# Kernel tuning notes

Measured on AMD Instinct MI355X. Metric: run time of the kernel, lower is better.

Reference implementation:

```python
import jax, jax.numpy as jnp
import numpy as np
from jax.scipy.linalg import expm

NUM_QUBITS = 10
D = 2 ** NUM_QUBITS  # 1024
B, S = 8, 4096


def setup_inputs() -> dict:
    key = jax.random.key(0)
    k_x, k_mr, k_mi = jax.random.split(key, 3)
    inputs = jax.random.normal(k_x, (B, S, D), dtype=jnp.float32)
    M_real = 0.1 * jax.random.normal(k_mr, (D, D), dtype=jnp.float32)
    M_imag = 0.1 * jax.random.normal(k_mi, (D, D), dtype=jnp.float32)
    bias = jnp.zeros((D,), dtype=jnp.float32)
    qubit_gate = jnp.ones((D,), dtype=jnp.float32)
    return {"inputs": inputs, "M_real": M_real, "M_imag": M_imag,
            "bias": bias, "qubit_gate": qubit_gate}


def _l2_normalize(x, axis=-1, eps=1e-12):
    # matches tf.linalg.l2_normalize: x * rsqrt(max(sum(x^2), eps))
    ss = jnp.sum(jnp.square(x), axis=axis, keepdims=True)
    return x * jax.lax.rsqrt(jnp.maximum(ss, eps))


def reference(inputs, M_real, M_imag, bias, qubit_gate):
    norm_inputs = _l2_normalize(inputs, axis=-1)
    A = M_real - M_real.T  # skew-symmetric -> expm(A) is orthogonal
    Bm = M_imag - M_imag.T
    U = expm(A) @ expm(Bm)  # [D, D]
    transformed = jnp.einsum('bsd,de->bse', norm_inputs, U) + bias
    measured = jnp.square(transformed)
    gate_probs = jax.nn.softmax(qubit_gate)  # [D]
    gated_output = measured * gate_probs
    return gated_output, gate_probs
```

## Files before the change

### kernel.cpp

```cpp
#include <hip/hip_runtime.h>


typedef unsigned int u32;
typedef unsigned short u16;
typedef __attribute__((ext_vector_type(8))) short short8;
typedef __attribute__((ext_vector_type(4))) float f32x4;

#define GLOBAL_AS __attribute__((address_space(1)))
#define LDS_AS    __attribute__((address_space(3)))

constexpr int D = 1024;
constexpr float EXPM_SCALE = 1.0f / 8.0f;

__device__ __forceinline__ u16 f2bf(float f) {
  union { float f; u32 u; } v; v.f = f;
  u32 r = (v.u + 0x7FFFu + ((v.u >> 16) & 1u)) >> 16;
  return (u16)r;
}
__device__ __forceinline__ float bf2f(u16 u) {
  union { u32 u; float f; } v; v.u = ((u32)u) << 16;
  return v.f;
}

__device__ __forceinline__ void g2l16(const void* g, void* l) {
  __builtin_amdgcn_global_load_lds((const GLOBAL_AS u32*)g, (LDS_AS u32*)l,
                                   16, 0, 0);
}

__device__ void norm_row(const float* __restrict__ x, u16* __restrict__ Xn,
                         int r, int tid, float* s4) {
  const float4 v = ((const float4*)(x + (size_t)r * D))[tid];
  float ss = v.x * v.x + v.y * v.y + v.z * v.z + v.w * v.w;
  for (int o = 32; o; o >>= 1) ss += __shfl_down(ss, o);
  if ((tid & 63) == 0) s4[tid >> 6] = ss;
  __syncthreads();
  const float tot = s4[0] + s4[1] + s4[2] + s4[3];
  const float inv = rsqrtf(fmaxf(tot, 1e-12f));
  ushort4 o4;
  o4.x = f2bf(v.x * inv); o4.y = f2bf(v.y * inv);
  o4.z = f2bf(v.z * inv); o4.w = f2bf(v.w * inv);
  ((ushort4*)(Xn + (size_t)r * D))[tid] = o4;
}

struct SkewParams {
  const float *Mr, *Mi;
  u16 *X0, *X1;
  const float* x;
  u16* Xn;
  int row0;
};
__global__ __launch_bounds__(256) void skew_norm_kernel(SkewParams p) {
  __shared__ __align__(16) float t2[64][67];
  const int bid = blockIdx.x, tid = threadIdx.x;
  if (bid >= 512) {
    norm_row(p.x, p.Xn, p.row0 + bid - 512, tid, &t2[0][0]);
    return;
  }
  const int z = bid >> 8, t = bid & 255;
  const float* M = z ? p.Mi : p.Mr;
  u16* X = z ? p.X1 : p.X0;
  const int bi = t >> 4, bj = t & 15;
  const int r0 = tid >> 4, c0 = (tid & 15) * 4;
  float4 own[4];
#pragma unroll
  for (int i = 0; i < 4; ++i) {
    const int r = i * 16 + r0;
    own[i] = *(const float4*)(M + (size_t)(bi * 64 + r) * D + bj * 64 + c0);
    const float4 tr =
        *(const float4*)(M + (size_t)(bj * 64 + r) * D + bi * 64 + c0);
    t2[r][c0 + 0] = tr.x; t2[r][c0 + 1] = tr.y;
    t2[r][c0 + 2] = tr.z; t2[r][c0 + 3] = tr.w;
  }
  __syncthreads();
#pragma unroll
  for (int i = 0; i < 4; ++i) {
    const int r = i * 16 + r0;
    const float o[4] = {own[i].x, own[i].y, own[i].z, own[i].w};
    ushort4 hv;
    u16* hp = (u16*)&hv;
#pragma unroll
    for (int j = 0; j < 4; ++j)
      hp[j] = f2bf((o[j] - t2[c0 + j][r]) * EXPM_SCALE);
    *(ushort4*)(X + (size_t)(bi * 64 + r) * D + bj * 64 + c0) = hv;
  }
}

struct CJob {
  const u16 *A, *B;
  const float* C;
  u16 *Dst, *DT;
  float alpha;
};
struct GNParams {
  CJob jobs[4];
  int njobs;
  const float* x;
  u16* Xn;
  int row0;
};
__global__ __launch_bounds__(256) void gemm_norm_kernel(GNParams p) {
  __shared__ __align__(16) u16 ldsA[2][64 * 64];
  __shared__ __align__(16) u16 ldsB[2][64 * 64];
  const int bid = blockIdx.x, tid = threadIdx.x;
  if (bid >= p.njobs) {
    norm_row(p.x, p.Xn, p.row0 + bid - p.njobs, tid, (float*)&ldsA[0][0]);
    return;
  }
  const CJob jb = p.jobs[bid >> 8];
  const int bi = (bid >> 4) & 15, bj = bid & 15;
  const int w = tid >> 6, lane = tid & 63;
  const int wr = w >> 1, wc = w & 1;
  f32x4 acc[2][2];
#pragma unroll
  for (int m = 0; m < 2; ++m)
#pragma unroll
    for (int n = 0; n < 2; ++n) acc[m][n] = f32x4{0.f, 0.f, 0.f, 0.f};
  const int r_l = lane >> 3, c_l = lane & 7;

  auto stage = [&](int buf, int kt) {
    const int k0 = kt * 64;
#pragma unroll
    for (int pp = 0; pp < 2; ++pp) {
      const int row = pp * 32 + w * 8 + r_l;
      const int chunk = c_l ^ (row & 7);
      g2l16(jb.A + (size_t)(bi * 64 + row) * D + k0 + chunk * 8,
            (char*)&ldsA[buf][0] + pp * 4096 + w * 1024);
      g2l16(jb.B + (size_t)(bj * 64 + row) * D + k0 + chunk * 8,
            (char*)&ldsB[buf][0] + pp * 4096 + w * 1024);
    }
  };

  stage(0, 0);
  __syncthreads();
  int buf = 0;
  for (int kt = 0; kt < 16; ++kt) {
    if (kt < 15) stage(buf ^ 1, kt + 1);
#pragma unroll
    for (int h = 0; h < 2; ++h) {
      const int kk = h * 32 + (lane >> 4) * 8;
      short8 a[2], b[2];
#pragma unroll
      for (int m = 0; m < 2; ++m) {
        const int row = wr * 32 + m * 16 + (lane & 15);
        const int off = row * 128 + ((kk * 2) ^ ((row & 7) << 4));
        a[m] = *(const short8*)((const char*)&ldsA[buf][0] + off);
      }
#pragma unroll
      for (int n = 0; n < 2; ++n) {
        const int row = wc * 32 + n * 16 + (lane & 15);
        const int off = row * 128 + ((kk * 2) ^ ((row & 7) << 4));
        b[n] = *(const short8*)((const char*)&ldsB[buf][0] + off);
      }
#pragma unroll
      for (int m = 0; m < 2; ++m)
#pragma unroll
        for (int n = 0; n < 2; ++n)
          acc[m][n] = __builtin_amdgcn_mfma_f32_16x16x32_bf16(
              a[m], b[n], acc[m][n], 0, 0, 0);
    }
    __syncthreads();
    buf ^= 1;
  }
  const int or0 = bi * 64 + wr * 32, oc0 = bj * 64 + wc * 32;
#pragma unroll
  for (int m = 0; m < 2; ++m)
#pragma unroll
    for (int n = 0; n < 2; ++n) {
      const int row0 = or0 + m * 16 + (lane >> 4) * 4;
      const int col = oc0 + n * 16 + (lane & 15);
      ushort4 dv;
      u16* dp = (u16*)&dv;
#pragma unroll
      for (int r = 0; r < 4; ++r) {
        float v = acc[m][n][r] * jb.alpha;
        if (jb.C) v += jb.C[(size_t)(row0 + r) * D + col];
        dp[r] = f2bf(v);
        jb.Dst[(size_t)(row0 + r) * D + col] = dp[r];
      }
      if (jb.DT)
        *(ushort4*)(jb.DT + (size_t)col * D + row0) = dv;
    }
}

struct BQParams {
  const u16 *X[2], *X2[2], *X3[2], *X4[2];
  float* q0[2];
  u16* q1t[2];
  const float* qg;
  float* gate_out;
  const float* x;
  u16* Xn;
  int row0;
};
__global__ __launch_bounds__(256) void buildq_norm_kernel(BQParams p) {
  __shared__ __align__(16) float red[16];
  const int bid = blockIdx.x, tid = threadIdx.x;
  if (bid > 512) {
    norm_row(p.x, p.Xn, p.row0 + bid - 513, tid, red);
    return;
  }
  if (bid == 512) {
    const float4 v = ((const float4*)p.qg)[tid];
    float mx = fmaxf(fmaxf(v.x, v.y), fmaxf(v.z, v.w));
#pragma unroll
    for (int o = 32; o; o >>= 1) mx = fmaxf(mx, __shfl_xor(mx, o));
    if ((tid & 63) == 0) red[tid >> 6] = mx;
    __syncthreads();
    const float M = fmaxf(fmaxf(red[0], red[1]), fmaxf(red[2], red[3]));
    __syncthreads();
    const float e0 = __expf(v.x - M), e1 = __expf(v.y - M),
                e2 = __expf(v.z - M), e3 = __expf(v.w - M);
    float s = e0 + e1 + e2 + e3;
#pragma unroll
    for (int o = 32; o; o >>= 1) s += __shfl_xor(s, o);
    if ((tid & 63) == 0) red[tid >> 6] = s;
    __syncthreads();
    const float S = red[0] + red[1] + red[2] + red[3];
    const float4 o4 = {e0 / S, e1 / S, e2 / S, e3 / S};
    ((float4*)p.gate_out)[tid] = o4;
    return;
  }
  const size_t idx0 = ((size_t)bid * 256 + tid) * 8;
  const int i = (int)(idx0 >> 10), j0 = (int)(idx0 & 1023);
#pragma unroll
  for (int m = 0; m < 2; ++m) {
    const short8 xv = *(const short8*)(p.X[m] + idx0);
    const short8 x2v = *(const short8*)(p.X2[m] + idx0);
    const short8 x3v = *(const short8*)(p.X3[m] + idx0);
    const short8 x4v = *(const short8*)(p.X4[m] + idx0);
    float q0o[8];
    short8 q1o;
#pragma unroll
    for (int k = 0; k < 8; ++k) {
      const float d = (i == (j0 + k)) ? 1.f : 0.f;
      const float x = bf2f((u16)xv[k]);
      const float x2 = bf2f((u16)x2v[k]);
      const float x3 = bf2f((u16)x3v[k]);
      const float x4 = bf2f((u16)x4v[k]);
      q0o[k] = d + x + x2 * 0.5f + x3 * (1.f / 6.f);
      q1o[k] = (short)f2bf(d * (1.f / 24.f) - x * (1.f / 120.f) +
                           x2 * (1.f / 720.f) - x3 * (1.f / 5040.f) +
                           x4 * (1.f / 40320.f));
    }
#pragma unroll
    for (int k = 0; k < 8; ++k) p.q0[m][idx0 + k] = q0o[k];
    *(short8*)(p.q1t[m] + idx0) = q1o;
  }
}

__global__ __launch_bounds__(512, 1) void main_gemm_kernel(
    const u16* __restrict__ Xn, const u16* __restrict__ Wm,
    const float* __restrict__ bias, const float* __restrict__ gate,
    float* __restrict__ out) {
  const int tid = threadIdx.x;
  const int wid = tid >> 6, lane = tid & 63;
  const int wr = wid >> 2, wc = wid & 3;
  __shared__ u16 ldsA[2][256 * 64];
  __shared__ u16 ldsB[2][256 * 64];
  f32x4 acc[8][4];
#pragma unroll
  for (int m = 0; m < 8; ++m)
#pragma unroll
    for (int n = 0; n < 4; ++n) acc[m][n] = f32x4{0.f, 0.f, 0.f, 0.f};

  const int bi = blockIdx.x, bj = blockIdx.y;
  const int r8 = tid >> 3;
  const int c_l = tid & 7;

  auto stage = [&](int buf, int kt) {
    const int k0 = kt * 64;
#pragma unroll
    for (int p = 0; p < 4; ++p) {
      const int row = p * 64 + r8;
      const int chunk = c_l ^ (row & 7);
      g2l16(Xn + (size_t)(bi * 256 + row) * D + k0 + chunk * 8,
            (u16*)((char*)&ldsA[buf][0] + p * 8192 + wid * 1024));
      g2l16(Wm + (size_t)(bj * 256 + row) * D + k0 + chunk * 8,
            (u16*)((char*)&ldsB[buf][0] + p * 8192 + wid * 1024));
    }
  };

  stage(0, 0);
  __syncthreads();
  int buf = 0;
  for (int kt = 0; kt < 16; ++kt) {
    if (kt < 15) stage(buf ^ 1, kt + 1);
#pragma unroll
    for (int ks = 0; ks < 2; ++ks) {
      const int kk = ks * 32 + (lane >> 4) * 8;
      short8 a[8], b[4];
#pragma unroll
      for (int m = 0; m < 8; ++m) {
        const int row = wr * 128 + m * 16 + (lane & 15);
        const int off = row * 128 + ((kk * 2) ^ ((row & 7) << 4));
        a[m] = *(const short8*)((const char*)&ldsA[buf][0] + off);
      }
#pragma unroll
      for (int n = 0; n < 4; ++n) {
        const int row = wc * 64 + n * 16 + (lane & 15);
        const int off = row * 128 + ((kk * 2) ^ ((row & 7) << 4));
        b[n] = *(const short8*)((const char*)&ldsB[buf][0] + off);
      }
      __builtin_amdgcn_s_setprio(1);
#pragma unroll
      for (int m = 0; m < 8; ++m)
#pragma unroll
        for (int n = 0; n < 4; ++n)
          acc[m][n] = __builtin_amdgcn_mfma_f32_16x16x32_bf16(
              a[m], b[n], acc[m][n], 0, 0, 0);
      __builtin_amdgcn_s_setprio(0);
    }
    __syncthreads();
    buf ^= 1;
  }
  const int or0 = bi * 256 + wr * 128, oc0 = bj * 256 + wc * 64;
#pragma unroll
  for (int m = 0; m < 8; ++m)
#pragma unroll
    for (int n = 0; n < 4; ++n) {
      const int col = oc0 + n * 16 + (lane & 15);
      const float bc = bias[col], gc = gate[col];
#pragma unroll
      for (int r = 0; r < 4; ++r) {
        const int row = or0 + m * 16 + (lane >> 4) * 4 + r;
        const float t = acc[m][n][r] + bc;
        out[(size_t)row * D + col] = t * t * gc;
      }
    }
}

extern "C" void kernel_launch(void* const* d_in, const int* in_sizes, int n_in,
                              void* d_out, int out_size, void* d_ws,
                              size_t ws_size, hipStream_t stream) {
  (void)in_sizes; (void)n_in; (void)out_size; (void)ws_size;
  const float* inp = (const float*)d_in[0];
  const float* Mr = (const float*)d_in[1];
  const float* Mi = (const float*)d_in[2];
  const float* bias = (const float*)d_in[3];
  const float* qg = (const float*)d_in[4];
  float* out = (float*)d_out;
  float* gate_out = out + (size_t)32768 * 1024;

  char* ws = (char*)d_ws;
  u16* Xn = (u16*)ws;
  auto slot = [&](int m, int s) -> u16* {
    return (u16*)(ws + 67108864 + (size_t)m * 16777216 + (size_t)s * 2097152);
  };
  auto q0p = [&](int m) -> float* {
    return (float*)(ws + 67108864 + (size_t)m * 16777216 + 12582912);
  };
  u16* W = (u16*)(ws + 100663296);

  const int CH = 3641;
  int row0 = 0;

  {
    SkewParams sp{Mr, Mi, slot(0, 0), slot(1, 0), inp, Xn, row0};
    skew_norm_kernel<<<512 + CH, 256, 0, stream>>>(sp);
    row0 += CH;
  }
  GNParams gp{};
  gp.x = inp; gp.Xn = Xn;
  for (int m = 0; m < 2; ++m)
    gp.jobs[m] = CJob{slot(m, 0), slot(m, 0), nullptr, slot(m, 1), nullptr,
                      -1.f};
  gp.njobs = 512; gp.row0 = row0;
  gemm_norm_kernel<<<512 + CH, 256, 0, stream>>>(gp);
  row0 += CH;
  for (int m = 0; m < 2; ++m) {
    gp.jobs[m * 2 + 0] = CJob{slot(m, 1), slot(m, 0), nullptr, slot(m, 2),
                              nullptr, -1.f};
    gp.jobs[m * 2 + 1] = CJob{slot(m, 1), slot(m, 1), nullptr, slot(m, 3),
                              nullptr, 1.f};
  }
  gp.njobs = 1024; gp.row0 = row0;
  gemm_norm_kernel<<<1024 + CH, 256, 0, stream>>>(gp);
  row0 += CH;
  {
    BQParams bq{};
    for (int m = 0; m < 2; ++m) {
      bq.X[m] = slot(m, 0); bq.X2[m] = slot(m, 1);
      bq.X3[m] = slot(m, 2); bq.X4[m] = slot(m, 3);
      bq.q0[m] = q0p(m); bq.q1t[m] = slot(m, 4);
    }
    bq.qg = qg; bq.gate_out = gate_out;
    bq.x = inp; bq.Xn = Xn; bq.row0 = row0;
    buildq_norm_kernel<<<513 + CH, 256, 0, stream>>>(bq);
    row0 += CH;
  }
  for (int m = 0; m < 2; ++m)
    gp.jobs[m] = CJob{slot(m, 3), slot(m, 4), q0p(m), slot(m, 0), slot(m, 1),
                      1.f};
  gp.njobs = 512; gp.row0 = row0;
  gemm_norm_kernel<<<512 + CH, 256, 0, stream>>>(gp);
  row0 += CH;
  for (int m = 0; m < 2; ++m)
    gp.jobs[m] = CJob{slot(m, 0), slot(m, 1), nullptr, slot(m, 2), slot(m, 4),
                      1.f};
  gp.row0 = row0;
  gemm_norm_kernel<<<512 + CH, 256, 0, stream>>>(gp);
  row0 += CH;
  for (int m = 0; m < 2; ++m)
    gp.jobs[m] = CJob{slot(m, 2), slot(m, 4), nullptr, slot(m, 3), slot(m, 5),
                      1.f};
  gp.row0 = row0;
  gemm_norm_kernel<<<512 + CH, 256, 0, stream>>>(gp);
  row0 += CH;
  for (int m = 0; m < 2; ++m)
    gp.jobs[m] = CJob{slot(m, 3), slot(m, 5), nullptr, slot(m, 0), slot(m, 1),
                      1.f};
  gp.row0 = row0;
  gemm_norm_kernel<<<512 + CH, 256, 0, stream>>>(gp);
  row0 += CH;
  gp.jobs[0] = CJob{slot(1, 1), slot(0, 0), nullptr, W, nullptr, 1.f};
  gp.njobs = 256; gp.row0 = row0;
  gemm_norm_kernel<<<256 + (32768 - row0), 256, 0, stream>>>(gp);

  main_gemm_kernel<<<dim3(128, 4), 512, 0, stream>>>(Xn, W, bias, gate_out,
                                                     out);
}
```

Measured before the change: 243.8 us.

## Batch norm rows, fuse X^3/X^4 GEMMs with Q build, deepen main GEMM pipeline

Each norm block now normalizes 8 rows instead of one, so the side work riding along each launch shrinks to 512 blocks. The separate X^3/X^4 GEMM launch and the elementwise Q-building kernel are merged into one kernel that shares the A tile across both products and builds q0/q1t in the epilogue. The main GEMM moves from a double-buffered 64-wide K tile to a four-stage 32-wide K ring with explicit vmcnt waits and raw barriers, aiming to overlap global loads with MFMA. This drops one launch and hides more load latency, but adds register and LDS pressure in the fused kernel and relies on hand-written wait counts being correct.

New measurement: 236.0 us. 1.03x faster.

```diff
diff --git a/kernel.cpp b/kernel.cpp
--- a/kernel.cpp
+++ b/kernel.cpp
@@ -27,19 +27,41 @@
                                    16, 0, 0);
 }
 
-__device__ void norm_row(const float* __restrict__ x, u16* __restrict__ Xn,
-                         int r, int tid, float* s4) {
-  const float4 v = ((const float4*)(x + (size_t)r * D))[tid];
-  float ss = v.x * v.x + v.y * v.y + v.z * v.z + v.w * v.w;
-  for (int o = 32; o; o >>= 1) ss += __shfl_down(ss, o);
-  if ((tid & 63) == 0) s4[tid >> 6] = ss;
+#define WAITV(N)                                                   \
+  do {                                                             \
+    asm volatile("s_waitcnt vmcnt(" #N ")" ::: "memory");          \
+    __builtin_amdgcn_sched_barrier(0);                             \
+  } while (0)
+
+__device__ void norm_rows8(const float* __restrict__ x, u16* __restrict__ Xn,
+                           int r0, int tid, float* sred) {
+  float4 v[8];
+#pragma unroll
+  for (int i = 0; i < 8; ++i)
+    v[i] = ((const float4*)(x + (size_t)(r0 + i) * D))[tid];
+  float ss[8];
+#pragma unroll
+  for (int i = 0; i < 8; ++i)
+    ss[i] = v[i].x * v[i].x + v[i].y * v[i].y + v[i].z * v[i].z +
+            v[i].w * v[i].w;
+  for (int o = 32; o; o >>= 1)
+#pragma unroll
+    for (int i = 0; i < 8; ++i) ss[i] += __shfl_down(ss[i], o);
+  const int w = tid >> 6;
+  if ((tid & 63) == 0)
+#pragma unroll
+    for (int i = 0; i < 8; ++i) sred[i * 4 + w] = ss[i];
   __syncthreads();
-  const float tot = s4[0] + s4[1] + s4[2] + s4[3];
-  const float inv = rsqrtf(fmaxf(tot, 1e-12f));
-  ushort4 o4;
-  o4.x = f2bf(v.x * inv); o4.y = f2bf(v.y * inv);
-  o4.z = f2bf(v.z * inv); o4.w = f2bf(v.w * inv);
-  ((ushort4*)(Xn + (size_t)r * D))[tid] = o4;
+#pragma unroll
+  for (int i = 0; i < 8; ++i) {
+    const float tot =
+        sred[i * 4 + 0] + sred[i * 4 + 1] + sred[i * 4 + 2] + sred[i * 4 + 3];
+    const float inv = rsqrtf(fmaxf(tot, 1e-12f));
+    ushort4 o4;
+    o4.x = f2bf(v[i].x * inv); o4.y = f2bf(v[i].y * inv);
+    o4.z = f2bf(v[i].z * inv); o4.w = f2bf(v[i].w * inv);
+    ((ushort4*)(Xn + (size_t)(r0 + i) * D))[tid] = o4;
+  }
 }
 
 struct SkewParams {
@@ -53,7 +75,7 @@
   __shared__ __align__(16) float t2[64][67];
   const int bid = blockIdx.x, tid = threadIdx.x;
   if (bid >= 512) {
-    norm_row(p.x, p.Xn, p.row0 + bid - 512, tid, &t2[0][0]);
+    norm_rows8(p.x, p.Xn, p.row0 + (bid - 512) * 8, tid, &t2[0][0]);
     return;
   }
   const int z = bid >> 8, t = bid & 255;
@@ -92,7 +114,7 @@
   float alpha;
 };
 struct GNParams {
-  CJob jobs[4];
+  CJob jobs[2];
   int njobs;
   const float* x;
   u16* Xn;
@@ -103,7 +125,8 @@
   __shared__ __align__(16) u16 ldsB[2][64 * 64];
   const int bid = blockIdx.x, tid = threadIdx.x;
   if (bid >= p.njobs) {
-    norm_row(p.x, p.Xn, p.row0 + bid - p.njobs, tid, (float*)&ldsA[0][0]);
+    norm_rows8(p.x, p.Xn, p.row0 + (bid - p.njobs) * 8, tid,
+               (float*)&ldsA[0][0]);
     return;
   }
   const CJob jb = p.jobs[bid >> 8];
@@ -182,27 +205,29 @@
     }
 }
 
-struct BQParams {
-  const u16 *X[2], *X2[2], *X3[2], *X4[2];
+struct X34Params {
+  const u16 *X[2], *X2[2];
+  u16 *X3[2], *X4[2], *q1t[2];
   float* q0[2];
-  u16* q1t[2];
   const float* qg;
   float* gate_out;
   const float* x;
   u16* Xn;
   int row0;
 };
-__global__ __launch_bounds__(256) void buildq_norm_kernel(BQParams p) {
-  __shared__ __align__(16) float red[16];
+__global__ __launch_bounds__(256) void x34q_norm_kernel(X34Params p) {
+  __shared__ __align__(16) u16 ldsA[2][64 * 64];
+  __shared__ __align__(16) u16 ldsB1[2][64 * 64];
+  __shared__ __align__(16) u16 ldsB2[2][64 * 64];
   const int bid = blockIdx.x, tid = threadIdx.x;
   if (bid > 512) {
-    norm_row(p.x, p.Xn, p.row0 + bid - 513, tid, red);
+    norm_rows8(p.x, p.Xn, p.row0 + (bid - 513) * 8, tid, (float*)&ldsA[0][0]);
     return;
   }
   if (bid == 512) {
+    float* red = (float*)&ldsA[0][0];
     const float4 v = ((const float4*)p.qg)[tid];
     float mx = fmaxf(fmaxf(v.x, v.y), fmaxf(v.z, v.w));
-#pragma unroll
     for (int o = 32; o; o >>= 1) mx = fmaxf(mx, __shfl_xor(mx, o));
     if ((tid & 63) == 0) red[tid >> 6] = mx;
     __syncthreads();
@@ -211,7 +236,6 @@
     const float e0 = __expf(v.x - M), e1 = __expf(v.y - M),
                 e2 = __expf(v.z - M), e3 = __expf(v.w - M);
     float s = e0 + e1 + e2 + e3;
-#pragma unroll
     for (int o = 32; o; o >>= 1) s += __shfl_xor(s, o);
     if ((tid & 63) == 0) red[tid >> 6] = s;
     __syncthreads();
@@ -220,32 +244,97 @@
     ((float4*)p.gate_out)[tid] = o4;
     return;
   }
-  const size_t idx0 = ((size_t)bid * 256 + tid) * 8;
-  const int i = (int)(idx0 >> 10), j0 = (int)(idx0 & 1023);
-#pragma unroll
-  for (int m = 0; m < 2; ++m) {
-    const short8 xv = *(const short8*)(p.X[m] + idx0);
-    const short8 x2v = *(const short8*)(p.X2[m] + idx0);
-    const short8 x3v = *(const short8*)(p.X3[m] + idx0);
-    const short8 x4v = *(const short8*)(p.X4[m] + idx0);
-    float q0o[8];
-    short8 q1o;
-#pragma unroll
-    for (int k = 0; k < 8; ++k) {
-      const float d = (i == (j0 + k)) ? 1.f : 0.f;
-      const float x = bf2f((u16)xv[k]);
-      const float x2 = bf2f((u16)x2v[k]);
-      const float x3 = bf2f((u16)x3v[k]);
-      const float x4 = bf2f((u16)x4v[k]);
-      q0o[k] = d + x + x2 * 0.5f + x3 * (1.f / 6.f);
-      q1o[k] = (short)f2bf(d * (1.f / 24.f) - x * (1.f / 120.f) +
-                           x2 * (1.f / 720.f) - x3 * (1.f / 5040.f) +
-                           x4 * (1.f / 40320.f));
-    }
-#pragma unroll
-    for (int k = 0; k < 8; ++k) p.q0[m][idx0 + k] = q0o[k];
-    *(short8*)(p.q1t[m] + idx0) = q1o;
-  }
+  const int mz = bid >> 8, t = bid & 255;
+  const int bi = t >> 4, bj = t & 15;
+  const u16* Ag = p.X2[mz];
+  const u16* B1g = p.X[mz];
+  const u16* B2g = p.X2[mz];
+  const int w = tid >> 6, lane = tid & 63;
+  const int wr = w >> 1, wc = w & 1;
+  f32x4 acc3[2][2], acc4[2][2];
+#pragma unroll
+  for (int m = 0; m < 2; ++m)
+#pragma unroll
+    for (int n = 0; n < 2; ++n) {
+      acc3[m][n] = f32x4{0.f, 0.f, 0.f, 0.f};
+      acc4[m][n] = f32x4{0.f, 0.f, 0.f, 0.f};
+    }
+  const int r_l = lane >> 3, c_l = lane & 7;
+
+  auto stage = [&](int buf, int kt) {
+    const int k0 = kt * 64;
+#pragma unroll
+    for (int pp = 0; pp < 2; ++pp) {
+      const int row = pp * 32 + w * 8 + r_l;
+      const int chunk = c_l ^ (row & 7);
+      g2l16(Ag + (size_t)(bi * 64 + row) * D + k0 + chunk * 8,
+            (char*)&ldsA[buf][0] + pp * 4096 + w * 1024);
+      g2l16(B1g + (size_t)(bj * 64 + row) * D + k0 + chunk * 8,
+            (char*)&ldsB1[buf][0] + pp * 4096 + w * 1024);
+      g2l16(B2g + (size_t)(bj * 64 + row) * D + k0 + chunk * 8,
+            (char*)&ldsB2[buf][0] + pp * 4096 + w * 1024);
+    }
+  };
+
+  stage(0, 0);
+  __syncthreads();
+  int buf = 0;
+  for (int kt = 0; kt < 16; ++kt) {
+    if (kt < 15) stage(buf ^ 1, kt + 1);
+#pragma unroll
+    for (int h = 0; h < 2; ++h) {
+      const int kk = h * 32 + (lane >> 4) * 8;
+      short8 a[2], b1[2], b2[2];
+#pragma unroll
+      for (int m = 0; m < 2; ++m) {
+        const int row = wr * 32 + m * 16 + (lane & 15);
+        const int off = row * 128 + ((kk * 2) ^ ((row & 7) << 4));
+        a[m] = *(const short8*)((const char*)&ldsA[buf][0] + off);
+      }
+#pragma unroll
+      for (int n = 0; n < 2; ++n) {
+        const int row = wc * 32 + n * 16 + (lane & 15);
+        const int off = row * 128 + ((kk * 2) ^ ((row & 7) << 4));
+        b1[n] = *(const short8*)((const char*)&ldsB1[buf][0] + off);
+        b2[n] = *(const short8*)((const char*)&ldsB2[buf][0] + off);
+      }
+#pragma unroll
+      for (int m = 0; m < 2; ++m)
+#pragma unroll
+        for (int n = 0; n < 2; ++n) {
+          acc3[m][n] = __builtin_amdgcn_mfma_f32_16x16x32_bf16(
+              a[m], b1[n], acc3[m][n], 0, 0, 0);
+          acc4[m][n] = __builtin_amdgcn_mfma_f32_16x16x32_bf16(
+              a[m], b2[n], acc4[m][n], 0, 0, 0);
+        }
+    }
+    __syncthreads();
+    buf ^= 1;
+  }
+  const int or0 = bi * 64 + wr * 32, oc0 = bj * 64 + wc * 32;
+#pragma unroll
+  for (int m = 0; m < 2; ++m)
+#pragma unroll
+    for (int n = 0; n < 2; ++n) {
+      const int row0 = or0 + m * 16 + (lane >> 4) * 4;
+      const int col = oc0 + n * 16 + (lane & 15);
+#pragma unroll
+      for (int r = 0; r < 4; ++r) {
+        const size_t idx = (size_t)(row0 + r) * D + col;
+        const u16 x3v = f2bf(-acc3[m][n][r]);
+        const u16 x4v = f2bf(acc4[m][n][r]);
+        p.X3[mz][idx] = x3v;
+        p.X4[mz][idx] = x4v;
+        const float d = (row0 + r == col) ? 1.f : 0.f;
+        const float xf = bf2f(p.X[mz][idx]);
+        const float x2f = bf2f(p.X2[mz][idx]);
+        const float x3f = bf2f(x3v), x4f = bf2f(x4v);
+        p.q0[mz][idx] = d + xf + x2f * 0.5f + x3f * (1.f / 6.f);
+        p.q1t[mz][idx] =
+            f2bf(d * (1.f / 24.f) - xf * (1.f / 120.f) + x2f * (1.f / 720.f) -
+                 x3f * (1.f / 5040.f) + x4f * (1.f / 40320.f));
+      }
+    }
 }
 
 __global__ __launch_bounds__(512, 1) void main_gemm_kernel(
@@ -255,8 +344,7 @@
   const int tid = threadIdx.x;
   const int wid = tid >> 6, lane = tid & 63;
   const int wr = wid >> 2, wc = wid & 3;
-  __shared__ u16 ldsA[2][256 * 64];
-  __shared__ u16 ldsB[2][256 * 64];
+  __shared__ u16 lds[4 * 16384];
   f32x4 acc[8][4];
 #pragma unroll
   for (int m = 0; m < 8; ++m)
@@ -264,55 +352,69 @@
     for (int n = 0; n < 4; ++n) acc[m][n] = f32x4{0.f, 0.f, 0.f, 0.f};
 
   const int bi = blockIdx.x, bj = blockIdx.y;
-  const int r8 = tid >> 3;
-  const int c_l = tid & 7;
-
-  auto stage = [&](int buf, int kt) {
-    const int k0 = kt * 64;
-#pragma unroll
-    for (int p = 0; p < 4; ++p) {
-      const int row = p * 64 + r8;
-      const int chunk = c_l ^ (row & 7);
-      g2l16(Xn + (size_t)(bi * 256 + row) * D + k0 + chunk * 8,
-            (u16*)((char*)&ldsA[buf][0] + p * 8192 + wid * 1024));
-      g2l16(Wm + (size_t)(bj * 256 + row) * D + k0 + chunk * 8,
-            (u16*)((char*)&ldsB[buf][0] + p * 8192 + wid * 1024));
+  const int r_ = tid >> 2;
+  const int c_ = tid & 3;
+
+  auto stage = [&](int s) {
+    char* base = (char*)lds + (s & 3) * 32768;
+#pragma unroll
+    for (int pp = 0; pp < 2; ++pp) {
+      const int row = pp * 128 + r_;
+      const int csrc = c_ ^ ((row >> 1) & 3);
+      g2l16(Xn + (size_t)(bi * 256 + row) * D + s * 32 + csrc * 8,
+            base + pp * 8192 + tid * 16);
+      g2l16(Wm + (size_t)(bj * 256 + row) * D + s * 32 + csrc * 8,
+            base + 16384 + pp * 8192 + tid * 16);
     }
   };
 
-  stage(0, 0);
-  __syncthreads();
-  int buf = 0;
-  for (int kt = 0; kt < 16; ++kt) {
-    if (kt < 15) stage(buf ^ 1, kt + 1);
-#pragma unroll
-    for (int ks = 0; ks < 2; ++ks) {
-      const int kk = ks * 32 + (lane >> 4) * 8;
-      short8 a[8], b[4];
-#pragma unroll
-      for (int m = 0; m < 8; ++m) {
-        const int row = wr * 128 + m * 16 + (lane & 15);
-        const int off = row * 128 + ((kk * 2) ^ ((row & 7) << 4));
-        a[m] = *(const short8*)((const char*)&ldsA[buf][0] + off);
-      }
-#pragma unroll
-      for (int n = 0; n < 4; ++n) {
-        const int row = wc * 64 + n * 16 + (lane & 15);
-        const int off = row * 128 + ((kk * 2) ^ ((row & 7) << 4));
-        b[n] = *(const short8*)((const char*)&ldsB[buf][0] + off);
-      }
-      __builtin_amdgcn_s_setprio(1);
-#pragma unroll
-      for (int m = 0; m < 8; ++m)
-#pragma unroll
-        for (int n = 0; n < 4; ++n)
-          acc[m][n] = __builtin_amdgcn_mfma_f32_16x16x32_bf16(
-              a[m], b[n], acc[m][n], 0, 0, 0);
-      __builtin_amdgcn_s_setprio(0);
-    }
-    __syncthreads();
-    buf ^= 1;
-  }
+  const int h = lane >> 4;
+  auto compute = [&](int s) {
+    const char* base = (const char*)lds + (s & 3) * 32768;
+    short8 a[8], b[4];
+#pragma unroll
+    for (int m = 0; m < 8; ++m) {
+      const int row = wr * 128 + m * 16 + (lane & 15);
+      const int off = row * 64 + ((h ^ ((row >> 1) & 3)) << 4);
+      a[m] = *(const short8*)(base + off);
+    }
+#pragma unroll
+    for (int n = 0; n < 4; ++n) {
+      const int row = wc * 64 + n * 16 + (lane & 15);
+      const int off = 16384 + row * 64 + ((h ^ ((row >> 1) & 3)) << 4);
+      b[n] = *(const short8*)(base + off);
+    }
+    __builtin_amdgcn_s_setprio(1);
+#pragma unroll
+    for (int m = 0; m < 8; ++m)
+#pragma unroll
+      for (int n = 0; n < 4; ++n)
+        acc[m][n] = __builtin_amdgcn_mfma_f32_16x16x32_bf16(a[m], b[n],
+                                                            acc[m][n], 0, 0, 0);
+    __builtin_amdgcn_s_setprio(0);
+  };
+
+  stage(0); stage(1); stage(2);
+  for (int s = 0; s < 29; ++s) {
+    WAITV(8);
+    __builtin_amdgcn_s_barrier();
+    __builtin_amdgcn_sched_barrier(0);
+    stage(s + 3);
+    compute(s);
+  }
+  WAITV(8);
+  __builtin_amdgcn_s_barrier();
+  __builtin_amdgcn_sched_barrier(0);
+  compute(29);
+  WAITV(4);
+  __builtin_amdgcn_s_barrier();
+  __builtin_amdgcn_sched_barrier(0);
+  compute(30);
+  WAITV(0);
+  __builtin_amdgcn_s_barrier();
+  __builtin_amdgcn_sched_barrier(0);
+  compute(31);
+
   const int or0 = bi * 256 + wr * 128, oc0 = bj * 256 + wc * 64;
 #pragma unroll
   for (int m = 0; m < 8; ++m)
@@ -351,12 +453,12 @@
   };
   u16* W = (u16*)(ws + 100663296);
 
-  const int CH = 3641;
+  const int CH = 4096, NB = 512;
   int row0 = 0;
 
   {
     SkewParams sp{Mr, Mi, slot(0, 0), slot(1, 0), inp, Xn, row0};
-    skew_norm_kernel<<<512 + CH, 256, 0, stream>>>(sp);
+    skew_norm_kernel<<<512 + NB, 256, 0, stream>>>(sp);
     row0 += CH;
   }
   GNParams gp{};
@@ -365,56 +467,47 @@
     gp.jobs[m] = CJob{slot(m, 0), slot(m, 0), nullptr, slot(m, 1), nullptr,
                       -1.f};
   gp.njobs = 512; gp.row0 = row0;
-  gemm_norm_kernel<<<512 + CH, 256, 0, stream>>>(gp);
-  row0 += CH;
-  for (int m = 0; m < 2; ++m) {
-    gp.jobs[m * 2 + 0] = CJob{slot(m, 1), slot(m, 0), nullptr, slot(m, 2),
-                              nullptr, -1.f};
-    gp.jobs[m * 2 + 1] = CJob{slot(m, 1), slot(m, 1), nullptr, slot(m, 3),
-                              nullptr, 1.f};
-  }
-  gp.njobs = 1024; gp.row0 = row0;
-  gemm_norm_kernel<<<1024 + CH, 256, 0, stream>>>(gp);
+  gemm_norm_kernel<<<512 + NB, 256, 0, stream>>>(gp);
   row0 += CH;
   {
-    BQParams bq{};
+    X34Params xp{};
     for (int m = 0; m < 2; ++m) {
-      bq.X[m] = slot(m, 0); bq.X2[m] = slot(m, 1);
-      bq.X3[m] = slot(m, 2); bq.X4[m] = slot(m, 3);
-      bq.q0[m] = q0p(m); bq.q1t[m] = slot(m, 4);
-    }
-    bq.qg = qg; bq.gate_out = gate_out;
-    bq.x = inp; bq.Xn = Xn; bq.row0 = row0;
-    buildq_norm_kernel<<<513 + CH, 256, 0, stream>>>(bq);
+      xp.X[m] = slot(m, 0); xp.X2[m] = slot(m, 1);
+      xp.X3[m] = slot(m, 2); xp.X4[m] = slot(m, 3);
+      xp.q1t[m] = slot(m, 4); xp.q0[m] = q0p(m);
+    }
+    xp.qg = qg; xp.gate_out = gate_out;
+    xp.x = inp; xp.Xn = Xn; xp.row0 = row0;
+    x34q_norm_kernel<<<513 + NB, 256, 0, stream>>>(xp);
     row0 += CH;
   }
   for (int m = 0; m < 2; ++m)
     gp.jobs[m] = CJob{slot(m, 3), slot(m, 4), q0p(m), slot(m, 0), slot(m, 1),
                       1.f};
   gp.njobs = 512; gp.row0 = row0;
-  gemm_norm_kernel<<<512 + CH, 256, 0, stream>>>(gp);
+  gemm_norm_kernel<<<512 + NB, 256, 0, stream>>>(gp);
   row0 += CH;
   for (int m = 0; m < 2; ++m)
     gp.jobs[m] = CJob{slot(m, 0), slot(m, 1), nullptr, slot(m, 2), slot(m, 4),
                       1.f};
   gp.row0 = row0;
-  gemm_norm_kernel<<<512 + CH, 256, 0, stream>>>(gp);
+  gemm_norm_kernel<<<512 + NB, 256, 0, stream>>>(gp);
   row0 += CH;
   for (int m = 0; m < 2; ++m)
     gp.jobs[m] = CJob{slot(m, 2), slot(m, 4), nullptr, slot(m, 3), slot(m, 5),
                       1.f};
   gp.row0 = row0;
-  gemm_norm_kernel<<<512 + CH, 256, 0, stream>>>(gp);
+  gemm_norm_kernel<<<512 + NB, 256, 0, stream>>>(gp);
   row0 += CH;
   for (int m = 0; m < 2; ++m)
     gp.jobs[m] = CJob{slot(m, 3), slot(m, 5), nullptr, slot(m, 0), slot(m, 1),
                       1.f};
   gp.row0 = row0;
-  gemm_norm_kernel<<<512 + CH, 256, 0, stream>>>(gp);
+  gemm_norm_kernel<<<512 + NB, 256, 0, stream>>>(gp);
   row0 += CH;
   gp.jobs[0] = CJob{slot(1, 1), slot(0, 0), nullptr, W, nullptr, 1.f};
   gp.njobs = 256; gp.row0 = row0;
-  gemm_norm_kernel<<<256 + (32768 - row0), 256, 0, stream>>>(gp);
+  gemm_norm_kernel<<<256 + NB, 256, 0, stream>>>(gp);
 
   main_gemm_kernel<<<dim3(128, 4), 512, 0, stream>>>(Xn, W, bias, gate_out,
                                                      out);
```
